# Kernel tuning notes

Measured on AMD Instinct MI355X. Metric: run time of the kernel, lower is better.

## Reference

```python
import jax, jax.numpy as jnp
import numpy as np

N_NODES = 50000
N_EDGES = 800000
NDIM_IN = 64
EDIMS = 64
NDIM_OUT = 128


def setup_inputs() -> dict:
    key = jax.random.key(0)
    k = jax.random.split(key, 8)
    nfeats = jax.random.normal(k[0], (N_NODES, NDIM_IN), dtype=jnp.float32)
    efeats = jax.random.normal(k[1], (N_EDGES, EDIMS), dtype=jnp.float32)
    # Linear weights stored as [in, out]; scaled for stable activations.
    W_msg = jax.random.normal(k[2], (NDIM_IN + EDIMS, NDIM_OUT), dtype=jnp.float32) * 0.05
    b_msg = jax.random.normal(k[3], (NDIM_OUT,), dtype=jnp.float32) * 0.05
    W_apply = jax.random.normal(k[4], (NDIM_IN + NDIM_OUT, NDIM_OUT), dtype=jnp.float32) * 0.05
    b_apply = jax.random.normal(k[5], (NDIM_OUT,), dtype=jnp.float32) * 0.05
    src = jax.random.randint(k[6], (N_EDGES,), 0, N_NODES, dtype=jnp.int64)
    dst = jax.random.randint(k[7], (N_EDGES,), 0, N_NODES, dtype=jnp.int64)
    return {
        "nfeats": nfeats,
        "efeats": efeats,
        "W_msg": W_msg,
        "b_msg": b_msg,
        "W_apply": W_apply,
        "b_apply": b_apply,
        "src": src,
        "dst": dst,
    }


def reference(nfeats, efeats, W_msg, b_msg, W_apply, b_apply, src, dst):
    # message: per-edge gather src node feats, concat with edge feats, linear+relu
    msg_in = jnp.concatenate([nfeats[src], efeats], axis=1)          # [E, ndim_in+edims]
    m = jax.nn.relu(msg_in @ W_msg + b_msg)                           # [E, ndim_out]
    # aggregate: sum messages into destination nodes
    h_neigh = jax.ops.segment_sum(m, dst, num_segments=nfeats.shape[0])  # [N, ndim_out]
    # update: concat original node feats with aggregated messages, linear+relu
    out = jax.nn.relu(jnp.concatenate([nfeats, h_neigh], axis=1) @ W_apply + b_apply)
    return out
```

## Files before the change

### kernel.cpp

```cpp
#include <hip/hip_runtime.h>
#include <hip/hip_bf16.h>

#define N_NODES  50000
#define N_EDGES  800000
#define NDIM_IN  64
#define EDIMS    64
#define NDIM_OUT 128

typedef __bf16 bf16;
typedef bf16  bf16x8 __attribute__((ext_vector_type(8)));
typedef float f32x4  __attribute__((ext_vector_type(4)));

__device__ __forceinline__ bool detect_f32(const void* nfeats) {
    const unsigned short* w = (const unsigned short*)nfeats;
    for (int i = 0; i < 64; i += 2) {
        const int e = (w[i] >> 7) & 0xFF;
        if (e < 100 || e > 134) return true;
    }
    return false;
}
__device__ __forceinline__ bool detect_i64(const int* p) {
    for (int i = 1; i < 64; i += 2) if (p[i] != 0) return false;
    return true;
}

__device__ __forceinline__ bf16x8 load8(const void* p, int off, bool f32) {
    if (f32) {
        const float* q = (const float*)p + off;
        const f32x4 a = *(const f32x4*)q;
        const f32x4 b = *(const f32x4*)(q + 4);
        bf16x8 r;
        #pragma unroll
        for (int u = 0; u < 4; ++u) { r[u] = (bf16)a[u]; r[4 + u] = (bf16)b[u]; }
        return r;
    }
    return *(const bf16x8*)((const bf16*)p + off);
}
__device__ __forceinline__ float loadf(const void* p, int i, bool f32) {
    return f32 ? ((const float*)p)[i] : (float)((const bf16*)p)[i];
}
__device__ __forceinline__ void storef(void* p, int i, float v, bool f32) {
    if (f32) ((float*)p)[i] = v; else ((bf16*)p)[i] = (bf16)v;
}

__global__ __launch_bounds__(256) void edge_msg_kernel(
    const void* __restrict__ nfeats,
    const void* __restrict__ efeats,
    const void* __restrict__ W_msg,
    const void* __restrict__ b_msg,
    const int*  __restrict__ src,
    const int*  __restrict__ dst,
    float*      __restrict__ h_neigh)
{
    __shared__ bf16 sWT[128 * 136];
    __shared__ int s_flags;

    const int tid = threadIdx.x;
    if (tid == 0)
        s_flags = (detect_f32(nfeats) ? 1 : 0) | (detect_i64(dst) ? 2 : 0);
    __syncthreads();
    const bool f32 = (s_flags & 1) != 0;
    const int  ish = (s_flags & 2) ? 1 : 0;

    #pragma unroll
    for (int it = 0; it < 8; ++it) {
        const int task = it * 256 + tid;
        const int k = task >> 4;
        const int c = task & 15;
        const bf16x8 w = load8(W_msg, k * 128 + c * 8, f32);
        #pragma unroll
        for (int u = 0; u < 8; ++u) sWT[(c * 8 + u) * 136 + k] = w[u];
    }
    __syncthreads();

    const int wave = tid >> 6;
    const int lane = tid & 63;
    const int m    = lane & 15;
    const int quad = lane >> 4;

    const int nchunks = N_EDGES / 64;
    for (int chunk = blockIdx.x; chunk < nchunks; chunk += gridDim.x) {
        const int ebase = chunk * 64 + wave * 16;
        const int e_m   = ebase + m;
        const int s     = src[e_m << ish];

        bf16x8 a[4];
        a[0] = load8(nfeats, s   * 64 +      quad * 8, f32);
        a[1] = load8(nfeats, s   * 64 + 32 + quad * 8, f32);
        a[2] = load8(efeats, e_m * 64 +      quad * 8, f32);
        a[3] = load8(efeats, e_m * 64 + 32 + quad * 8, f32);

        int drow[4];
        #pragma unroll
        for (int i = 0; i < 4; ++i)
            drow[i] = dst[(ebase + quad * 4 + i) << ish] * 128;

        #pragma unroll
        for (int t = 0; t < 8; ++t) {
            f32x4 acc = {0.f, 0.f, 0.f, 0.f};
            const bf16* bp = sWT + (t * 16 + m) * 136 + quad * 8;
            #pragma unroll
            for (int kb = 0; kb < 4; ++kb)
                acc = __builtin_amdgcn_mfma_f32_16x16x32_bf16(
                          a[kb], *(const bf16x8*)(bp + kb * 32), acc, 0, 0, 0);
            const int   n    = t * 16 + m;
            const float bias = loadf(b_msg, n, f32);
            #pragma unroll
            for (int i = 0; i < 4; ++i) {
                float v = acc[i] + bias;
                v = v > 0.f ? v : 0.f;
                unsafeAtomicAdd(h_neigh + drow[i] + n, v);
            }
        }
    }
}

__global__ __launch_bounds__(256) void apply_kernel(
    const void*  __restrict__ nfeats,
    const float* __restrict__ h_neigh,
    const void*  __restrict__ W_apply,
    const void*  __restrict__ b_apply,
    void*        __restrict__ out)
{
    __shared__ bf16 sWT[128 * 200];
    __shared__ int s_flags;

    const int tid = threadIdx.x;
    if (tid == 0) s_flags = detect_f32(nfeats) ? 1 : 0;
    __syncthreads();
    const bool f32 = (s_flags & 1) != 0;

    #pragma unroll
    for (int it = 0; it < 12; ++it) {
        const int task = it * 256 + tid;
        const int k = task >> 4;
        const int c = task & 15;
        const bf16x8 w = load8(W_apply, k * 128 + c * 8, f32);
        #pragma unroll
        for (int u = 0; u < 8; ++u) sWT[(c * 8 + u) * 200 + k] = w[u];
    }
    __syncthreads();

    const int wave = tid >> 6;
    const int lane = tid & 63;
    const int m    = lane & 15;
    const int quad = lane >> 4;

    const int nchunks = (N_NODES + 63) / 64;
    for (int chunk = blockIdx.x; chunk < nchunks; chunk += gridDim.x) {
        const int nbase = chunk * 64 + wave * 16;
        const int nm  = nbase + m;
        const int nmc = nm < N_NODES ? nm : N_NODES - 1;

        bf16x8 a[6];
        a[0] = load8(nfeats, nmc * 64 +      quad * 8, f32);
        a[1] = load8(nfeats, nmc * 64 + 32 + quad * 8, f32);
        #pragma unroll
        for (int kb = 0; kb < 4; ++kb) {
            const float* hp = h_neigh + nmc * 128 + kb * 32 + quad * 8;
            const f32x4 p = *(const f32x4*)(hp);
            const f32x4 q = *(const f32x4*)(hp + 4);
            bf16x8 r;
            #pragma unroll
            for (int u = 0; u < 4; ++u) { r[u] = (bf16)p[u]; r[4 + u] = (bf16)q[u]; }
            a[2 + kb] = r;
        }

        #pragma unroll
        for (int t = 0; t < 8; ++t) {
            f32x4 acc = {0.f, 0.f, 0.f, 0.f};
            const bf16* bp = sWT + (t * 16 + m) * 200 + quad * 8;
            #pragma unroll
            for (int kb = 0; kb < 6; ++kb)
                acc = __builtin_amdgcn_mfma_f32_16x16x32_bf16(
                          a[kb], *(const bf16x8*)(bp + kb * 32), acc, 0, 0, 0);
            const int   n    = t * 16 + m;
            const float bias = loadf(b_apply, n, f32);
            #pragma unroll
            for (int i = 0; i < 4; ++i) {
                const int row = nbase + quad * 4 + i;
                if (row < N_NODES) {
                    float v = acc[i] + bias;
                    v = v > 0.f ? v : 0.f;
                    storef(out, row * 128 + n, v, f32);
                }
            }
        }
    }
}

extern "C" void kernel_launch(void* const* d_in, const int* in_sizes, int n_in,
                              void* d_out, int out_size, void* d_ws, size_t ws_size,
                              hipStream_t stream) {
    const void* nfeats  = d_in[0];
    const void* efeats  = d_in[1];
    const void* W_msg   = d_in[2];
    const void* b_msg   = d_in[3];
    const void* W_apply = d_in[4];
    const void* b_apply = d_in[5];
    const int*  src     = (const int*)d_in[6];
    const int*  dst     = (const int*)d_in[7];
    float*      h_neigh = (float*)d_ws;

    hipMemsetAsync(h_neigh, 0, (size_t)N_NODES * NDIM_OUT * sizeof(float), stream);

    edge_msg_kernel<<<768, 256, 0, stream>>>(nfeats, efeats, W_msg, b_msg, src, dst, h_neigh);
    apply_kernel<<<512, 256, 0, stream>>>(nfeats, h_neigh, W_apply, b_apply, d_out);
}
```

Baseline: 665.5 us.

## Replace atomic scatter aggregation with CSR-sorted per-destination message reduction

Builds a CSR grouping of edges by destination (histogram, single-block scan, atomic-cursor scatter) and then has one wave per destination node compute that node's messages with MFMA and reduce them in registers, writing h_neigh once without atomics. This removes the roughly 100M float atomic adds and the memset of h_neigh. In exchange it adds three preprocessing kernels, including a serial single-block scan, and edge features are now read gathered by edge id, in effectively random order. Low-degree nodes also waste part of each 16-row MFMA tile.

Result: slower. 680.9 us (+2.3%).

```diff
diff --git a/kernel.cpp b/kernel.cpp
--- a/kernel.cpp
+++ b/kernel.cpp
@@ -41,6 +41,160 @@
 }
 __device__ __forceinline__ void storef(void* p, int i, float v, bool f32) {
     if (f32) ((float*)p)[i] = v; else ((bf16*)p)[i] = (bf16)v;
+}
+
+__global__ __launch_bounds__(256) void hist_kernel(const int* __restrict__ dst,
+                                                   int* __restrict__ cnt) {
+    __shared__ int s_ish;
+    if (threadIdx.x == 0) s_ish = detect_i64(dst) ? 1 : 0;
+    __syncthreads();
+    const int ish = s_ish;
+    const int stride = gridDim.x * blockDim.x;
+    for (int e = blockIdx.x * blockDim.x + threadIdx.x; e < N_EDGES; e += stride)
+        atomicAdd(&cnt[dst[e << ish]], 1);
+}
+
+__global__ __launch_bounds__(1024) void scan_kernel(int* __restrict__ cnt,
+                                                    int* __restrict__ row_ptr) {
+    __shared__ int sp[1024];
+    const int t = threadIdx.x;
+    const int PER = 49;
+    const int base = t * PER;
+    int s = 0;
+    for (int j = 0; j < PER; ++j) {
+        const int i = base + j;
+        if (i < N_NODES) s += cnt[i];
+    }
+    sp[t] = s;
+    __syncthreads();
+    for (int off = 1; off < 1024; off <<= 1) {
+        const int v = (t >= off) ? sp[t - off] : 0;
+        __syncthreads();
+        sp[t] += v;
+        __syncthreads();
+    }
+    int run = sp[t] - s;
+    for (int j = 0; j < PER; ++j) {
+        const int i = base + j;
+        if (i < N_NODES) {
+            const int c = cnt[i];
+            row_ptr[i] = run;
+            cnt[i] = run;
+            run += c;
+        }
+    }
+    if (t == 0) row_ptr[N_NODES] = N_EDGES;
+}
+
+__global__ __launch_bounds__(256) void scatter_kernel(const int* __restrict__ src,
+                                                      const int* __restrict__ dst,
+                                                      int* __restrict__ cursor,
+                                                      int* __restrict__ eid,
+                                                      int* __restrict__ srcs) {
+    __shared__ int s_ish;
+    if (threadIdx.x == 0) s_ish = detect_i64(dst) ? 1 : 0;
+    __syncthreads();
+    const int ish = s_ish;
+    const int stride = gridDim.x * blockDim.x;
+    for (int e = blockIdx.x * blockDim.x + threadIdx.x; e < N_EDGES; e += stride) {
+        const int d = dst[e << ish];
+        const int pos = atomicAdd(&cursor[d], 1);
+        eid[pos]  = e;
+        srcs[pos] = src[e << ish];
+    }
+}
+
+__global__ __launch_bounds__(256) void msg_agg_kernel(
+    const void* __restrict__ nfeats,
+    const void* __restrict__ efeats,
+    const void* __restrict__ W_msg,
+    const void* __restrict__ b_msg,
+    const int*  __restrict__ row_ptr,
+    const int*  __restrict__ eid,
+    const int*  __restrict__ srcs,
+    float*      __restrict__ h_neigh)
+{
+    __shared__ bf16 sWT[128 * 136];
+    __shared__ int s_flags;
+
+    const int tid = threadIdx.x;
+    if (tid == 0) s_flags = detect_f32(nfeats) ? 1 : 0;
+    __syncthreads();
+    const bool f32 = (s_flags & 1) != 0;
+
+    #pragma unroll
+    for (int it = 0; it < 8; ++it) {
+        const int task = it * 256 + tid;
+        const int k = task >> 4;
+        const int c = task & 15;
+        const bf16x8 w = load8(W_msg, k * 128 + c * 8, f32);
+        #pragma unroll
+        for (int u = 0; u < 8; ++u) sWT[(c * 8 + u) * 136 + k] = w[u];
+    }
+    __syncthreads();
+
+    const int wave = tid >> 6;
+    const int lane = tid & 63;
+    const int m    = lane & 15;
+    const int quad = lane >> 4;
+
+    float bias[8];
+    #pragma unroll
+    for (int t = 0; t < 8; ++t) bias[t] = loadf(b_msg, t * 16 + m, f32);
+
+    const int wstride = gridDim.x * 4;
+    for (int v = blockIdx.x * 4 + wave; v < N_NODES; v += wstride) {
+        const int beg = row_ptr[v];
+        const int deg = row_ptr[v + 1] - beg;
+
+        float hacc[8] = {0.f, 0.f, 0.f, 0.f, 0.f, 0.f, 0.f, 0.f};
+
+        for (int T = 0; T * 16 < deg; ++T) {
+            const int r0 = T * 16;
+            const int sl = (r0 + m < deg) ? (beg + r0 + m) : beg;
+            const int s  = srcs[sl];
+            const int e  = eid[sl];
+
+            bf16x8 a[4];
+            a[0] = load8(nfeats, s * 64 +      quad * 8, f32);
+            a[1] = load8(nfeats, s * 64 + 32 + quad * 8, f32);
+            a[2] = load8(efeats, e * 64 +      quad * 8, f32);
+            a[3] = load8(efeats, e * 64 + 32 + quad * 8, f32);
+
+            #pragma unroll
+            for (int t = 0; t < 8; ++t) {
+                f32x4 acc = {0.f, 0.f, 0.f, 0.f};
+                const bf16* bp = sWT + (t * 16 + m) * 136 + quad * 8;
+                #pragma unroll
+                for (int kb = 0; kb < 4; ++kb)
+                    acc = __builtin_amdgcn_mfma_f32_16x16x32_bf16(
+                              a[kb], *(const bf16x8*)(bp + kb * 32), acc, 0, 0, 0);
+                float part = 0.f;
+                #pragma unroll
+                for (int i = 0; i < 4; ++i) {
+                    float val = acc[i] + bias[t];
+                    val = val > 0.f ? val : 0.f;
+                    if (r0 + quad * 4 + i < deg) part += val;
+                }
+                hacc[t] += part;
+            }
+        }
+
+        #pragma unroll
+        for (int t = 0; t < 8; ++t) {
+            float s = hacc[t];
+            s += __shfl_xor(s, 16, 64);
+            s += __shfl_xor(s, 32, 64);
+            hacc[t] = s;
+        }
+
+        const float lo = quad < 2 ? (quad == 0 ? hacc[0] : hacc[1])
+                                  : (quad == 2 ? hacc[2] : hacc[3]);
+        const float hi = quad < 2 ? (quad == 0 ? hacc[4] : hacc[5])
+                                  : (quad == 2 ? hacc[6] : hacc[7]);
+        h_neigh[v * 128 + lane]      = lo;
+        h_neigh[v * 128 + 64 + lane] = hi;
+    }
 }
 
 __global__ __launch_bounds__(256) void edge_msg_kernel(
@@ -200,10 +354,32 @@
     const void* b_apply = d_in[5];
     const int*  src     = (const int*)d_in[6];
     const int*  dst     = (const int*)d_in[7];
-    float*      h_neigh = (float*)d_ws;
-
-    hipMemsetAsync(h_neigh, 0, (size_t)N_NODES * NDIM_OUT * sizeof(float), stream);
-
-    edge_msg_kernel<<<768, 256, 0, stream>>>(nfeats, efeats, W_msg, b_msg, src, dst, h_neigh);
+
+    float* h_neigh = (float*)d_ws;
+
+    const size_t OFF_ROWPTR = 25600000;
+    const size_t OFF_CNT    = OFF_ROWPTR + 200064;
+    const size_t OFF_EID    = OFF_CNT + 200064;
+    const size_t OFF_SRCS   = OFF_EID + 3200000;
+    const size_t NEED       = OFF_SRCS + 3200000;
+
+    if (ws_size >= NEED) {
+        int* row_ptr = (int*)((char*)d_ws + OFF_ROWPTR);
+        int* cnt     = (int*)((char*)d_ws + OFF_CNT);
+        int* eid     = (int*)((char*)d_ws + OFF_EID);
+        int* srcs    = (int*)((char*)d_ws + OFF_SRCS);
+
+        hipMemsetAsync(cnt, 0, (size_t)N_NODES * sizeof(int), stream);
+        hist_kernel<<<1024, 256, 0, stream>>>(dst, cnt);
+        scan_kernel<<<1, 1024, 0, stream>>>(cnt, row_ptr);
+        scatter_kernel<<<1024, 256, 0, stream>>>(src, dst, cnt, eid, srcs);
+        msg_agg_kernel<<<1024, 256, 0, stream>>>(nfeats, efeats, W_msg, b_msg,
+                                                 row_ptr, eid, srcs, h_neigh);
+    } else {
+        hipMemsetAsync(h_neigh, 0, (size_t)N_NODES * NDIM_OUT * sizeof(float), stream);
+        edge_msg_kernel<<<768, 256, 0, stream>>>(nfeats, efeats, W_msg, b_msg,
+                                                 src, dst, h_neigh);
+    }
+
     apply_kernel<<<512, 256, 0, stream>>>(nfeats, h_neigh, W_apply, b_apply, d_out);
 }
```
